# Optimization experiments

Hardware: AMD Instinct MI355X
Metric: run time of the kernel (lower is better)

The kernel has to match this reference:

```python
import jax, jax.numpy as jnp
import numpy as np

D_IN = 4096
D_OUT = 4096
TOKENS = 8192


def setup_inputs() -> dict:
    key = jax.random.key(0)
    k_x, k_w = jax.random.split(key)
    x = jax.random.normal(k_x, (TOKENS, D_IN), dtype=jnp.float32)
    # int8 weight buffer (stored as int32 for jax friendliness; values in [-128,127))
    weight_i8 = jax.random.randint(k_w, (D_OUT, D_IN), -128, 127, dtype=jnp.int32)
    return {
        "x": x,
        "weight_i8": weight_i8,
        "weight_scale": jnp.array([0.01], dtype=jnp.float32),
        "weight_zero_point": jnp.zeros((1,), dtype=jnp.int32),
        "bias": jnp.zeros((D_OUT,), dtype=jnp.float32),
        "output_scale": jnp.array([0.5], dtype=jnp.float32),
        "output_zero_point": jnp.full((1,), 128, dtype=jnp.int32),
    }


def reference(x, weight_i8, weight_scale, weight_zero_point, bias,
              output_scale, output_zero_point):
    # NOTE: the torch module also computes torch.quantize_per_tensor(x, ...)
    # whose result is unused (dead code); it does not affect the output and
    # is omitted here.
    # Dequantize int8 weight: (w_int - zp) * scale  -> [D_OUT, D_IN] fp32
    w = (weight_i8.astype(jnp.float32)
         - weight_zero_point.astype(jnp.float32)) * weight_scale
    # Standard fp32 linear: [T, D_IN] @ [D_IN, D_OUT] + bias
    out = jnp.einsum("ti,oi->to", x, w) + bias
    # quantize_per_tensor(out, output_scale, output_zp, quint8).dequantize():
    # q = clamp(round(out/scale) + zp, 0, 255); deq = (q - zp) * scale
    zp = output_zero_point.astype(jnp.float32)
    q = jnp.clip(jnp.round(out / output_scale) + zp, 0.0, 255.0)
    return (q - zp) * output_scale
```

## Files before the change

kernel.cpp:

```cpp
#include <hip/hip_runtime.h>

#define TOKENS 8192
#define D_IN   4096
#define D_OUT  4096

typedef _Float16 f16;
typedef __attribute__((ext_vector_type(8))) _Float16 half8;
typedef __attribute__((ext_vector_type(4))) float    f32x4;
typedef __attribute__((address_space(3))) char       lds_char;


__global__ void cvt_x_kernel(const float* __restrict__ x, f16* __restrict__ xh) {
    size_t i = ((size_t)blockIdx.x * blockDim.x + threadIdx.x) * 4;
    float4 v = *reinterpret_cast<const float4*>(x + i);
    union { f16 h[4]; uint2 u; } p;
    p.h[0] = (f16)v.x; p.h[1] = (f16)v.y; p.h[2] = (f16)v.z; p.h[3] = (f16)v.w;
    *reinterpret_cast<uint2*>(xh + i) = p.u;
}

__global__ void cvt_w_kernel(const int* __restrict__ w, f16* __restrict__ wh,
                             const float* __restrict__ scale_p,
                             const int* __restrict__ zp_p) {
    size_t i = ((size_t)blockIdx.x * blockDim.x + threadIdx.x) * 4;
    float s = scale_p[0];
    float z = (float)zp_p[0];
    int4 v = *reinterpret_cast<const int4*>(w + i);
    union { f16 h[4]; uint2 u; } p;
    p.h[0] = (f16)(((float)v.x - z) * s);
    p.h[1] = (f16)(((float)v.y - z) * s);
    p.h[2] = (f16)(((float)v.z - z) * s);
    p.h[3] = (f16)(((float)v.w - z) * s);
    *reinterpret_cast<uint2*>(wh + i) = p.u;
}


#define BM 256
#define BN 128
#define BK 32
#define NT (D_IN / BK)
#define LDS_BUF   24576
#define LDS_B_OFF 16384

__device__ __forceinline__ void stage16(const f16* g, lds_char* l) {
    __builtin_amdgcn_global_load_lds(
        (const __attribute__((address_space(1))) void*)g,
        (__attribute__((address_space(3))) void*)l, 16, 0, 0);
}

#define LDS_LOAD8(p) (*(const __attribute__((address_space(3))) half8*)(p))

#define BAR()      __builtin_amdgcn_s_barrier()
#define LGKM0()    asm volatile("s_waitcnt lgkmcnt(0)" ::: "memory")
#define VMCNT0()   asm volatile("s_waitcnt vmcnt(0)" ::: "memory")
#define PRIO(x)    __builtin_amdgcn_s_setprio(x)

__global__ __launch_bounds__(512, 4)
void gemm_occ(const f16* __restrict__ A, const f16* __restrict__ B,
              const float* __restrict__ bias,
              const float* __restrict__ oscale_p, const int* __restrict__ ozp_p,
              float* __restrict__ C)
{
    __shared__ __align__(1024) char smem_[2 * LDS_BUF];
    lds_char* smem = (lds_char*)smem_;
    constexpr int K = D_IN, N = D_OUT;

    int nwg = gridDim.x;
    int cpx = nwg >> 3;
    int bid = blockIdx.x;
    int swz = (bid & 7) * cpx + (bid >> 3);
    int ntn = N / BN;
    int m0 = (swz / ntn) * BM;
    int n0 = (swz % ntn) * BN;

    int tid = threadIdx.x;
    int l   = tid & 63;
    int wv  = tid >> 6;
    int wr  = wv >> 1;
    int wc  = wv & 1;
    int lr  = l & 15;

    int srow = wv * 16 + (l >> 2);
    int scol = ((l & 3) ^ ((srow >> 1) & 3)) * 8;
    const f16* gA = A + (size_t)(m0 + srow) * K + scol;
    const f16* gB = B + (size_t)(n0 + srow) * K + scol;
    lds_char* dstbase = smem + wv * 1024 + l * 16;

    int colsel = ((l >> 4) ^ ((lr >> 1) & 3)) << 4;
    int aoff = (wr * 64 + lr) * 64 + colsel;
    int boff = LDS_B_OFF + (wc * 64 + lr) * 64 + colsel;

    f32x4 acc[4][4] = {};
    half8 a[4], b[4];

    stage16(gA,                    dstbase);
    stage16(gA + (size_t)128 * K,  dstbase + 8192);
    stage16(gB,                    dstbase + LDS_B_OFF);
    VMCNT0();
    BAR();

    for (int t = 0; t < NT - 1; ++t) {
        const lds_char* bufr = smem + (t & 1) * LDS_BUF;
        lds_char* dstw = dstbase + ((t + 1) & 1) * LDS_BUF;
        const f16* nA = gA + (size_t)(t + 1) * BK;
        const f16* nB = gB + (size_t)(t + 1) * BK;

        stage16(nA,                   dstw);
        stage16(nA + (size_t)128 * K, dstw + 8192);
        stage16(nB,                   dstw + LDS_B_OFF);

        #pragma unroll
        for (int fm = 0; fm < 4; ++fm) a[fm] = LDS_LOAD8(bufr + aoff + fm * 1024);
        #pragma unroll
        for (int fn = 0; fn < 4; ++fn) b[fn] = LDS_LOAD8(bufr + boff + fn * 1024);

        PRIO(1);
        #pragma unroll
        for (int fm = 0; fm < 4; ++fm)
            #pragma unroll
            for (int fn = 0; fn < 4; ++fn)
                acc[fm][fn] = __builtin_amdgcn_mfma_f32_16x16x32_f16(
                    a[fm], b[fn], acc[fm][fn], 0, 0, 0);
        PRIO(0);

        LGKM0();
        VMCNT0();
        BAR();
    }

    {
        const lds_char* bufr = smem + ((NT - 1) & 1) * LDS_BUF;
        #pragma unroll
        for (int fm = 0; fm < 4; ++fm) a[fm] = LDS_LOAD8(bufr + aoff + fm * 1024);
        #pragma unroll
        for (int fn = 0; fn < 4; ++fn) b[fn] = LDS_LOAD8(bufr + boff + fn * 1024);
        PRIO(1);
        #pragma unroll
        for (int fm = 0; fm < 4; ++fm)
            #pragma unroll
            for (int fn = 0; fn < 4; ++fn)
                acc[fm][fn] = __builtin_amdgcn_mfma_f32_16x16x32_f16(
                    a[fm], b[fn], acc[fm][fn], 0, 0, 0);
        PRIO(0);
    }

    float os  = oscale_p[0];
    float ozp = (float)ozp_p[0];
    float inv = 1.0f / os;
    #pragma unroll
    for (int fm = 0; fm < 4; ++fm) {
        int rowb = m0 + wr * 64 + fm * 16 + (l >> 4) * 4;
        #pragma unroll
        for (int fn = 0; fn < 4; ++fn) {
            int col = n0 + wc * 64 + fn * 16 + lr;
            float bv = bias[col];
            f32x4 v = acc[fm][fn];
            #pragma unroll
            for (int j = 0; j < 4; ++j) {
                float o = v[j] + bv;
                float q = rintf(o * inv) + ozp;
                q = fminf(fmaxf(q, 0.0f), 255.0f);
                C[(size_t)(rowb + j) * N + col] = (q - ozp) * os;
            }
        }
    }
}


extern "C" void kernel_launch(void* const* d_in, const int* in_sizes, int n_in,
                              void* d_out, int out_size, void* d_ws, size_t ws_size,
                              hipStream_t stream) {
    const float* x      = (const float*)d_in[0];
    const int*   w8     = (const int*)d_in[1];
    const float* wscale = (const float*)d_in[2];
    const int*   wzp    = (const int*)d_in[3];
    const float* bias   = (const float*)d_in[4];
    const float* oscale = (const float*)d_in[5];
    const int*   ozp    = (const int*)d_in[6];
    float* out = (float*)d_out;

    const size_t x_elems = (size_t)TOKENS * D_IN;
    const size_t w_elems = (size_t)D_OUT * D_IN;
    const size_t need = (x_elems + w_elems) * sizeof(f16);
    if (ws_size < need) return;

    f16* xh = (f16*)d_ws;
    f16* wh = xh + x_elems;

    {
        int blocks = (int)(x_elems / 4 / 256);
        cvt_x_kernel<<<blocks, 256, 0, stream>>>(x, xh);
    }
    {
        int blocks = (int)(w_elems / 4 / 256);
        cvt_w_kernel<<<blocks, 256, 0, stream>>>(w8, wh, wscale, wzp);
    }
    {
        int grid = (TOKENS / BM) * (D_OUT / BN);
        gemm_occ<<<grid, 512, 0, stream>>>(xh, wh, bias, oscale, ozp, out);
    }
}
```

Before: 342.1 us.

## Enlarge GEMM tile to 256x256x64 with B fragments loaded directly into registers

Replaces the 256x128x32 GEMM with a 256x256x64 tile. Only A is staged through LDS; each wave loads its B fragments straight from global memory into registers, double-buffered across iterations. The main loop is unrolled by two with interleaved LDS reads and MFMA clusters, and uses partial vmcnt waits to overlap prefetch with compute. The aim is more data reuse per byte loaded and less LDS traffic, at the cost of higher register pressure (occupancy hint lowered to 2) and uncoalesced direct global B loads.

```diff
diff --git a/kernel.cpp b/kernel.cpp
--- a/kernel.cpp
+++ b/kernel.cpp
@@ -35,11 +35,10 @@
 
 
 #define BM 256
-#define BN 128
-#define BK 32
+#define BN 256
+#define BK 64
 #define NT (D_IN / BK)
-#define LDS_BUF   24576
-#define LDS_B_OFF 16384
+#define LDS_A 32768
 
 __device__ __forceinline__ void stage16(const f16* g, lds_char* l) {
     __builtin_amdgcn_global_load_lds(
@@ -49,18 +48,69 @@
 
 #define LDS_LOAD8(p) (*(const __attribute__((address_space(3))) half8*)(p))
 
+#define LOAD_AQ(DST, PIMM, QIMM)                                            \
+    do { _Pragma("unroll")                                                  \
+        for (int mq = 0; mq < 2; ++mq) {                                    \
+            DST[mq][0] = LDS_LOAD8(abase0 + (PIMM) + (QIMM) + mq * 2048);   \
+            DST[mq][1] = LDS_LOAD8(abase1 + (PIMM) + (QIMM) + mq * 2048);   \
+        } } while (0)
+
+#define CLUST(Q, AV, BV)                                                    \
+    do { _Pragma("unroll")                                                  \
+        for (int mq = 0; mq < 2; ++mq)                                      \
+            _Pragma("unroll")                                               \
+            for (int fn = 0; fn < 4; ++fn)                                  \
+                _Pragma("unroll")                                           \
+                for (int ks = 0; ks < 2; ++ks)                              \
+                    acc[(Q)*2+mq][fn] =                                     \
+                        __builtin_amdgcn_mfma_f32_16x16x32_f16(             \
+                            AV[mq][ks], BV[fn][ks],                         \
+                            acc[(Q)*2+mq][fn], 0, 0, 0);                    \
+    } while (0)
+
+#define FENCE()    asm volatile("" ::: "memory")
 #define BAR()      __builtin_amdgcn_s_barrier()
-#define LGKM0()    asm volatile("s_waitcnt lgkmcnt(0)" ::: "memory")
-#define VMCNT0()   asm volatile("s_waitcnt vmcnt(0)" ::: "memory")
+#define VMCNT(N)   asm volatile("s_waitcnt vmcnt(" #N ")" ::: "memory")
 #define PRIO(x)    __builtin_amdgcn_s_setprio(x)
 
-__global__ __launch_bounds__(512, 4)
-void gemm_occ(const f16* __restrict__ A, const f16* __restrict__ B,
-              const float* __restrict__ bias,
-              const float* __restrict__ oscale_p, const int* __restrict__ ozp_p,
-              float* __restrict__ C)
+#define TILE_BODY(TNEXT, PIMM, DSTW, BC, BN_, FULL)                         \
+    do {                                                                    \
+        VMCNT(8);                                          \
+        BAR();                                                              \
+        LOAD_AQ(aqa, PIMM, 0);                                     \
+        if (FULL) {                                                         \
+            const f16* sA = gA + (size_t)(TNEXT) * BK;                      \
+            stage16(sA,                    DSTW);                           \
+            stage16(sA + (size_t)64  * K,  (DSTW) + 8192);                  \
+            stage16(sA + (size_t)128 * K,  (DSTW) + 16384);                 \
+            stage16(sA + (size_t)192 * K,  (DSTW) + 24576);                 \
+            FENCE();                                        \
+            _Pragma("unroll")                                               \
+            for (int fn = 0; fn < 4; ++fn)                                  \
+                _Pragma("unroll")                                           \
+                for (int ks = 0; ks < 2; ++ks)                              \
+                    BN_[fn][ks] = *reinterpret_cast<const half8*>(          \
+                        gB4[fn] + (size_t)(TNEXT) * BK + ks * 32);          \
+            VMCNT(12);                                     \
+        } else {                                                            \
+            VMCNT(0);                                       \
+        }                                                                   \
+        LOAD_AQ(aqb, PIMM, 4096);                                  \
+        PRIO(1); CLUST(0, aqa, BC); PRIO(0);                                \
+        LOAD_AQ(aqa, PIMM, 8192);                                  \
+        PRIO(1); CLUST(1, aqb, BC); PRIO(0);                                \
+        LOAD_AQ(aqb, PIMM, 12288);                                 \
+        PRIO(1); CLUST(2, aqa, BC); PRIO(0);                                \
+        PRIO(1); CLUST(3, aqb, BC); PRIO(0);                                \
+    } while (0)
+
+__global__ __launch_bounds__(512, 2)
+void gemm_breg(const f16* __restrict__ A, const f16* __restrict__ B,
+               const float* __restrict__ bias,
+               const float* __restrict__ oscale_p, const int* __restrict__ ozp_p,
+               float* __restrict__ C)
 {
-    __shared__ __align__(1024) char smem_[2 * LDS_BUF];
+    __shared__ __align__(1024) char smem_[2 * LDS_A];
     lds_char* smem = (lds_char*)smem_;
     constexpr int K = D_IN, N = D_OUT;
 
@@ -68,92 +118,68 @@
     int cpx = nwg >> 3;
     int bid = blockIdx.x;
     int swz = (bid & 7) * cpx + (bid >> 3);
-    int ntn = N / BN;
-    int m0 = (swz / ntn) * BM;
-    int n0 = (swz % ntn) * BN;
+    int m0 = (swz & 31) * BM;
+    int n0 = (swz >> 5) * BN;
 
     int tid = threadIdx.x;
     int l   = tid & 63;
     int wv  = tid >> 6;
-    int wr  = wv >> 1;
-    int wc  = wv & 1;
+    int wr  = wv >> 2;
+    int wc  = wv & 3;
     int lr  = l & 15;
 
-    int srow = wv * 16 + (l >> 2);
-    int scol = ((l & 3) ^ ((srow >> 1) & 3)) * 8;
+    int srow = wv * 8 + (l >> 3);
+    int scol = ((l & 7) ^ (l >> 3)) * 8;
     const f16* gA = A + (size_t)(m0 + srow) * K + scol;
-    const f16* gB = B + (size_t)(n0 + srow) * K + scol;
-    lds_char* dstbase = smem + wv * 1024 + l * 16;
-
-    int colsel = ((l >> 4) ^ ((lr >> 1) & 3)) << 4;
-    int aoff = (wr * 64 + lr) * 64 + colsel;
-    int boff = LDS_B_OFF + (wc * 64 + lr) * 64 + colsel;
-
-    f32x4 acc[4][4] = {};
-    half8 a[4], b[4];
-
-    stage16(gA,                    dstbase);
-    stage16(gA + (size_t)128 * K,  dstbase + 8192);
-    stage16(gB,                    dstbase + LDS_B_OFF);
-    VMCNT0();
+    lds_char* dst0 = smem + wv * 1024 + l * 16;
+    lds_char* dst1 = dst0 + LDS_A;
+
+    int cb0  = (l >> 4) * 16;
+    int swzr = (l & 7) << 4;
+    int c0   = cb0 ^ swzr;
+    lds_char* abase0 = smem + (wr * 128 + lr) * 128 + c0;
+    lds_char* abase1 = smem + (wr * 128 + lr) * 128 + (c0 ^ 64);
+
+    const f16* gB4[4];
+    #pragma unroll
+    for (int fn = 0; fn < 4; ++fn)
+        gB4[fn] = B + (size_t)(n0 + wc * 64 + fn * 16 + lr) * K + (l >> 4) * 8;
+
+    f32x4 acc[8][4] = {};
+    half8 aqa[2][2], aqb[2][2];
+    half8 bE[4][2], bO[4][2];
+
+    stage16(gA,                   dst0);
+    stage16(gA + (size_t)64  * K, dst0 + 8192);
+    stage16(gA + (size_t)128 * K, dst0 + 16384);
+    stage16(gA + (size_t)192 * K, dst0 + 24576);
+    FENCE();
+    #pragma unroll
+    for (int fn = 0; fn < 4; ++fn)
+        #pragma unroll
+        for (int ks = 0; ks < 2; ++ks)
+            bE[fn][ks] = *reinterpret_cast<const half8*>(gB4[fn] + ks * 32);
+    VMCNT(0);
     BAR();
 
-    for (int t = 0; t < NT - 1; ++t) {
-        const lds_char* bufr = smem + (t & 1) * LDS_BUF;
-        lds_char* dstw = dstbase + ((t + 1) & 1) * LDS_BUF;
-        const f16* nA = gA + (size_t)(t + 1) * BK;
-        const f16* nB = gB + (size_t)(t + 1) * BK;
-
-        stage16(nA,                   dstw);
-        stage16(nA + (size_t)128 * K, dstw + 8192);
-        stage16(nB,                   dstw + LDS_B_OFF);
-
-        #pragma unroll
-        for (int fm = 0; fm < 4; ++fm) a[fm] = LDS_LOAD8(bufr + aoff + fm * 1024);
-        #pragma unroll
-        for (int fn = 0; fn < 4; ++fn) b[fn] = LDS_LOAD8(bufr + boff + fn * 1024);
-
-        PRIO(1);
-        #pragma unroll
-        for (int fm = 0; fm < 4; ++fm)
-            #pragma unroll
-            for (int fn = 0; fn < 4; ++fn)
-                acc[fm][fn] = __builtin_amdgcn_mfma_f32_16x16x32_f16(
-                    a[fm], b[fn], acc[fm][fn], 0, 0, 0);
-        PRIO(0);
-
-        LGKM0();
-        VMCNT0();
-        BAR();
-    }
-
-    {
-        const lds_char* bufr = smem + ((NT - 1) & 1) * LDS_BUF;
-        #pragma unroll
-        for (int fm = 0; fm < 4; ++fm) a[fm] = LDS_LOAD8(bufr + aoff + fm * 1024);
-        #pragma unroll
-        for (int fn = 0; fn < 4; ++fn) b[fn] = LDS_LOAD8(bufr + boff + fn * 1024);
-        PRIO(1);
-        #pragma unroll
-        for (int fm = 0; fm < 4; ++fm)
-            #pragma unroll
-            for (int fn = 0; fn < 4; ++fn)
-                acc[fm][fn] = __builtin_amdgcn_mfma_f32_16x16x32_f16(
-                    a[fm], b[fn], acc[fm][fn], 0, 0, 0);
-        PRIO(0);
-    }
+    for (int t = 0; t < NT - 2; t += 2) {
+        TILE_BODY(t + 1, 0,     dst1, bE, bO, true);
+        TILE_BODY(t + 2, 32768, dst0, bO, bE, true);
+    }
+    TILE_BODY(63, 0,     dst1, bE, bO, true);
+    TILE_BODY(64, 32768, dst0, bO, bE, false);
 
     float os  = oscale_p[0];
     float ozp = (float)ozp_p[0];
     float inv = 1.0f / os;
     #pragma unroll
-    for (int fm = 0; fm < 4; ++fm) {
-        int rowb = m0 + wr * 64 + fm * 16 + (l >> 4) * 4;
+    for (int mf = 0; mf < 8; ++mf) {
+        int rowb = m0 + wr * 128 + mf * 16 + (l >> 4) * 4;
         #pragma unroll
         for (int fn = 0; fn < 4; ++fn) {
             int col = n0 + wc * 64 + fn * 16 + lr;
             float bv = bias[col];
-            f32x4 v = acc[fm][fn];
+            f32x4 v = acc[mf][fn];
             #pragma unroll
             for (int j = 0; j < 4; ++j) {
                 float o = v[j] + bv;
@@ -196,6 +222,6 @@
     }
     {
         int grid = (TOKENS / BM) * (D_OUT / BN);
-        gemm_occ<<<grid, 512, 0, stream>>>(xh, wh, bias, oscale, ozp, out);
-    }
-}
+        gemm_breg<<<grid, 512, 0, stream>>>(xh, wh, bias, oscale, ozp, out);
+    }
+}
```

New measurement: 403.8 us. +18.0%, slower.

## Enlarge GEMM tile to 256x256 with four-stage LDS prefetch pipeline

Applied to the files above, without the earlier changes.

Doubles the N tile so each workgroup computes a 256x256 output block with 8x4 MFMA fragments per wave, raising data reuse per LDS load. Replaces the double buffer with a four-buffer ring that keeps three tiles in flight, waiting on partial vmcnt instead of draining all loads each iteration. Uses 128KB of LDS and 128 accumulator floats per thread, which caps residency at one block per CU and risks register pressure.

```diff
diff --git a/kernel.cpp b/kernel.cpp
--- a/kernel.cpp
+++ b/kernel.cpp
@@ -35,11 +35,11 @@
 
 
 #define BM 256
-#define BN 128
+#define BN 256
 #define BK 32
 #define NT (D_IN / BK)
-#define LDS_BUF   24576
-#define LDS_B_OFF 16384
+#define BUFSZ 32768
+#define B_OFF 16384
 
 __device__ __forceinline__ void stage16(const f16* g, lds_char* l) {
     __builtin_amdgcn_global_load_lds(
@@ -50,17 +50,45 @@
 #define LDS_LOAD8(p) (*(const __attribute__((address_space(3))) half8*)(p))
 
 #define BAR()      __builtin_amdgcn_s_barrier()
-#define LGKM0()    asm volatile("s_waitcnt lgkmcnt(0)" ::: "memory")
-#define VMCNT0()   asm volatile("s_waitcnt vmcnt(0)" ::: "memory")
+#define VMCNT(N)   asm volatile("s_waitcnt vmcnt(" #N ")" ::: "memory")
 #define PRIO(x)    __builtin_amdgcn_s_setprio(x)
 
-__global__ __launch_bounds__(512, 4)
-void gemm_occ(const f16* __restrict__ A, const f16* __restrict__ B,
-              const float* __restrict__ bias,
-              const float* __restrict__ oscale_p, const int* __restrict__ ozp_p,
-              float* __restrict__ C)
+#define READS_AND_MFMA(BUF)                                                 \
+    do {                                                                    \
+        _Pragma("unroll")                                                   \
+        for (int fm = 0; fm < 8; ++fm)                                      \
+            a[fm] = LDS_LOAD8((BUF) + aoff + fm * 1024);                    \
+        _Pragma("unroll")                                                   \
+        for (int fn = 0; fn < 4; ++fn)                                      \
+            b[fn] = LDS_LOAD8((BUF) + boff + fn * 1024);                    \
+        PRIO(1);                                                            \
+        _Pragma("unroll")                                                   \
+        for (int fm = 0; fm < 8; ++fm)                                      \
+            _Pragma("unroll")                                               \
+            for (int fn = 0; fn < 4; ++fn)                                  \
+                acc[fm][fn] = __builtin_amdgcn_mfma_f32_16x16x32_f16(       \
+                    a[fm], b[fn], acc[fm][fn], 0, 0, 0);                    \
+        PRIO(0);                                                            \
+    } while (0)
+
+#define STAGE_TILE(TT)                                                      \
+    do {                                                                    \
+        lds_char* dst = dstbase + ((TT) & 3) * BUFSZ;                       \
+        const f16* sA = gA + (size_t)(TT) * BK;                             \
+        const f16* sB = gB + (size_t)(TT) * BK;                             \
+        stage16(sA,                    dst);                                \
+        stage16(sA + (size_t)128 * K,  dst + 8192);                         \
+        stage16(sB,                    dst + B_OFF);                        \
+        stage16(sB + (size_t)128 * K,  dst + B_OFF + 8192);                 \
+    } while (0)
+
+__global__ __launch_bounds__(512, 2)
+void gemm_dp(const f16* __restrict__ A, const f16* __restrict__ B,
+             const float* __restrict__ bias,
+             const float* __restrict__ oscale_p, const int* __restrict__ ozp_p,
+             float* __restrict__ C)
 {
-    __shared__ __align__(1024) char smem_[2 * LDS_BUF];
+    __shared__ __align__(1024) char smem_[4 * BUFSZ];
     lds_char* smem = (lds_char*)smem_;
     constexpr int K = D_IN, N = D_OUT;
 
@@ -75,8 +103,8 @@
     int tid = threadIdx.x;
     int l   = tid & 63;
     int wv  = tid >> 6;
-    int wr  = wv >> 1;
-    int wc  = wv & 1;
+    int wr  = wv >> 2;
+    int wc  = wv & 3;
     int lr  = l & 15;
 
     int srow = wv * 16 + (l >> 2);
@@ -86,69 +114,41 @@
     lds_char* dstbase = smem + wv * 1024 + l * 16;
 
     int colsel = ((l >> 4) ^ ((lr >> 1) & 3)) << 4;
-    int aoff = (wr * 64 + lr) * 64 + colsel;
-    int boff = LDS_B_OFF + (wc * 64 + lr) * 64 + colsel;
-
-    f32x4 acc[4][4] = {};
-    half8 a[4], b[4];
-
-    stage16(gA,                    dstbase);
-    stage16(gA + (size_t)128 * K,  dstbase + 8192);
-    stage16(gB,                    dstbase + LDS_B_OFF);
-    VMCNT0();
+    int aoff = (wr * 128 + lr) * 64 + colsel;
+    int boff = B_OFF + (wc * 64 + lr) * 64 + colsel;
+
+    f32x4 acc[8][4] = {};
+    half8 a[8], b[4];
+
+    STAGE_TILE(0);
+    STAGE_TILE(1);
+    STAGE_TILE(2);
+    VMCNT(8);
     BAR();
 
-    for (int t = 0; t < NT - 1; ++t) {
-        const lds_char* bufr = smem + (t & 1) * LDS_BUF;
-        lds_char* dstw = dstbase + ((t + 1) & 1) * LDS_BUF;
-        const f16* nA = gA + (size_t)(t + 1) * BK;
-        const f16* nB = gB + (size_t)(t + 1) * BK;
-
-        stage16(nA,                   dstw);
-        stage16(nA + (size_t)128 * K, dstw + 8192);
-        stage16(nB,                   dstw + LDS_B_OFF);
-
-        #pragma unroll
-        for (int fm = 0; fm < 4; ++fm) a[fm] = LDS_LOAD8(bufr + aoff + fm * 1024);
-        #pragma unroll
-        for (int fn = 0; fn < 4; ++fn) b[fn] = LDS_LOAD8(bufr + boff + fn * 1024);
-
-        PRIO(1);
-        #pragma unroll
-        for (int fm = 0; fm < 4; ++fm)
-            #pragma unroll
-            for (int fn = 0; fn < 4; ++fn)
-                acc[fm][fn] = __builtin_amdgcn_mfma_f32_16x16x32_f16(
-                    a[fm], b[fn], acc[fm][fn], 0, 0, 0);
-        PRIO(0);
-
-        LGKM0();
-        VMCNT0();
+    for (int t = 0; t < NT - 3; ++t) {
+        const lds_char* buf = smem + (t & 3) * BUFSZ;
+        STAGE_TILE(t + 3);
+        READS_AND_MFMA(buf);
+        VMCNT(8);
         BAR();
     }
-
-    {
-        const lds_char* bufr = smem + ((NT - 1) & 1) * LDS_BUF;
-        #pragma unroll
-        for (int fm = 0; fm < 4; ++fm) a[fm] = LDS_LOAD8(bufr + aoff + fm * 1024);
-        #pragma unroll
-        for (int fn = 0; fn < 4; ++fn) b[fn] = LDS_LOAD8(bufr + boff + fn * 1024);
-        PRIO(1);
-        #pragma unroll
-        for (int fm = 0; fm < 4; ++fm)
-            #pragma unroll
-            for (int fn = 0; fn < 4; ++fn)
-                acc[fm][fn] = __builtin_amdgcn_mfma_f32_16x16x32_f16(
-                    a[fm], b[fn], acc[fm][fn], 0, 0, 0);
-        PRIO(0);
+    {
+        READS_AND_MFMA(smem + ((NT - 3) & 3) * BUFSZ);
+        VMCNT(4);
+        BAR();
+        READS_AND_MFMA(smem + ((NT - 2) & 3) * BUFSZ);
+        VMCNT(0);
+        BAR();
+        READS_AND_MFMA(smem + ((NT - 1) & 3) * BUFSZ);
     }
 
     float os  = oscale_p[0];
     float ozp = (float)ozp_p[0];
     float inv = 1.0f / os;
     #pragma unroll
-    for (int fm = 0; fm < 4; ++fm) {
-        int rowb = m0 + wr * 64 + fm * 16 + (l >> 4) * 4;
+    for (int fm = 0; fm < 8; ++fm) {
+        int rowb = m0 + wr * 128 + fm * 16 + (l >> 4) * 4;
         #pragma unroll
         for (int fn = 0; fn < 4; ++fn) {
             int col = n0 + wc * 64 + fn * 16 + lr;
@@ -196,6 +196,6 @@
     }
     {
         int grid = (TOKENS / BM) * (D_OUT / BN);
-        gemm_occ<<<grid, 512, 0, stream>>>(xh, wh, bias, oscale, ozp, out);
-    }
-}
+        gemm_dp<<<grid, 512, 0, stream>>>(xh, wh, bias, oscale, ozp, out);
+    }
+}
```

New measurement: 292.4 us. 14.5% less time.
